# Optimization experiments

Measured on AMD Instinct MI355X. Metric: run time of the kernel, lower is better.

Reference implementation:

```python
import jax, jax.numpy as jnp
import numpy as np

B, CIN, COUT, H, W, K = 32, 256, 256, 56, 56, 3
STRIDE, PAD, DIL = 1, 1, 1
SPARSITY = 0.9  # fraction of weight entries pruned to zero


def setup_inputs() -> dict:
    key = jax.random.key(0)
    kx, kw, km = jax.random.split(key, 3)
    x = jax.random.normal(kx, (B, CIN, H, W), dtype=jnp.float32)
    w = jax.random.normal(kw, (COUT, CIN, K, K), dtype=jnp.float32)
    mask = (jax.random.uniform(km, (COUT, CIN, K, K)) > SPARSITY).astype(jnp.float32)
    w = w * mask
    return {"x": x, "weight": w}


def reference(x, weight):
    # Faithful math of SparseConv2D.forward (sparse path == nn.Conv2d, bias=None):
    # NCHW input, OIHW weight, stride/pad/dilation as configured.
    out = jax.lax.conv_general_dilated(
        x, weight,
        window_strides=(STRIDE, STRIDE),
        padding=[(PAD, PAD), (PAD, PAD)],
        rhs_dilation=(DIL, DIL),
        dimension_numbers=("NCHW", "OIHW", "NCHW"),
    )
    return out  # [B, COUT, H_out, W_out]
```

## Files before the change

### kernel.cpp

```cpp
#include <hip/hip_runtime.h>


typedef __attribute__((ext_vector_type(8))) short short8;
typedef __attribute__((ext_vector_type(4))) float f32x4;
typedef __attribute__((ext_vector_type(4))) int i32x4;

constexpr int BB = 32, CIN = 256, COUT = 256, H = 56, W = 56, HW = H * W;
constexpr int HP = 58, WP = 58;

constexpr size_t XP_ELEMS = (size_t)BB * HP * WP * CIN;
constexpr size_t WB_ELEMS = (size_t)COUT * 9 * CIN;
constexpr size_t WS_NEEDED = (XP_ELEMS + WB_ELEMS) * 2;

__device__ __forceinline__ ushort f2bf(float f) {
    unsigned x = __float_as_uint(f);
    unsigned r = (x + 0x7FFFu + ((x >> 16) & 1u)) >> 16;
    return (ushort)r;
}


__global__ __launch_bounds__(256)
void prep_xp(const float* __restrict__ x, ushort* __restrict__ xp) {
    const int bi = blockIdx.x;
    const int b = bi / HP, i = bi % HP;
    ushort* dst = xp + (size_t)bi * WP * CIN;
    const int tid = threadIdx.x;

    if (i == 0 || i == HP - 1) {
        i32x4 z = {0, 0, 0, 0};
        for (int k = tid; k < WP * CIN / 8; k += 256) ((i32x4*)dst)[k] = z;
        return;
    }

    __shared__ ushort t[W][CIN + 2];
    const int lane = tid & 63, wv = tid >> 6;
    if (lane < W) {
        const float* src = x + (size_t)b * CIN * HW + (size_t)(i - 1) * W + lane;
        for (int cin = wv; cin < CIN; cin += 4)
            t[lane][cin] = f2bf(src[(size_t)cin * HW]);
    }
    __syncthreads();
    for (int c = 0; c < WP; ++c)
        dst[c * CIN + tid] = (c == 0 || c == WP - 1) ? (ushort)0 : t[c - 1][tid];
}

__global__ __launch_bounds__(256)
void prep_wb2(const float* __restrict__ w, ushort* __restrict__ wb2) {
    const int d = blockIdx.x * 256 + threadIdx.x;
    const int ci = d & 31;
    const int cout = (d >> 5) & 255;
    const int r = d >> 13;
    const int tap = r % 9, cb = r / 9;
    const int cin = cb * 32 + ci;
    wb2[d] = f2bf(w[((size_t)cout * CIN + cin) * 9 + tap]);
}


#define SCHED_FENCE() __builtin_amdgcn_sched_barrier(0)
#define WAITV(N) asm volatile("s_waitcnt vmcnt(" #N ")" ::: "memory")

__device__ __forceinline__ void gload_lds16(const ushort* g, ushort* l) {
    __builtin_amdgcn_global_load_lds(
        (const __attribute__((address_space(1))) void*)g,
        (__attribute__((address_space(3))) void*)l, 16, 0, 0);
}


__global__ __launch_bounds__(256, 2)
void conv_mfma(const ushort* __restrict__ xp, const ushort* __restrict__ wb2,
               float* __restrict__ out) {
    int bx = blockIdx.x;
    bx = (bx & 7) * 112 + (bx >> 3);

    const int b  = bx / 28;
    const int p0 = (bx % 28) * 112;
    const int r0 = p0 / 56;

    const int tid  = threadIdx.x;
    const int wv   = tid >> 6;
    const int lane = tid & 63;
    const int ml   = lane & 15;
    const int g    = lane >> 4;

    __shared__ ushort As[2][1280 * 8];
    __shared__ ushort Xs[2][1280 * 8];

    int boff[7];
    #pragma unroll
    for (int nf = 0; nf < 7; ++nf) {
        const int p_  = p0 + nf * 16 + ml;
        const int hl  = (p_ >= p0 + 56) ? 1 : 0;
        const int col = p_ - 56 * (r0 + hl);
        boff[nf] = (hl * 58 + col) * 40 + 8 * g;
    }
    int aoff[4];
    #pragma unroll
    for (int mi = 0; mi < 4; ++mi)
        aoff[mi] = (64 * wv + 16 * mi + ml) * 40 + 8 * g;

    int goffA[5], goffX[5];
    #pragma unroll
    for (int k = 0; k < 5; ++k) {
        const int c = 256 * k + tid;
        const int s = c / 5, pc = c - s * 5;
        goffA[k] = (pc < 4) ? s * 32 + pc * 8 : 0;
        goffX[k] = (c < 1160 && pc < 4) ? s * 256 + pc * 8 : 0;
    }
    const size_t xbase = ((size_t)b * HP + r0) * WP * CIN;

    f32x4 acc[4][7] = {};

    #define STAGE_A(T, BUF)                                                     \
        { const ushort* _s = wb2 + (size_t)(T) * 8192;                          \
          _Pragma("unroll")                                                     \
          for (int k = 0; k < 5; ++k)                                           \
              gload_lds16(_s + goffA[k], &As[BUF][(256 * k + 64 * wv) * 8]);    \
        }
    #define STAGE_X(CB, BUF)                                                    \
        { const ushort* _s = xp + xbase + (CB) * 32;                            \
          _Pragma("unroll")                                                     \
          for (int k = 0; k < 5; ++k)                                           \
              gload_lds16(_s + goffX[k], &Xs[BUF][(256 * k + 64 * wv) * 8]);    \
        }

    STAGE_A(0, 0);
    STAGE_A(1, 1);
    STAGE_X(0, 0);
    WAITV(0);
    __builtin_amdgcn_s_barrier();

    #pragma unroll
    for (int cb = 0; cb < 8; ++cb) {
        #pragma unroll
        for (int tap = 0; tap < 9; ++tap) {
            const int t = cb * 9 + tap;

            if (t == 71)                      { WAITV(0); }
            else if (tap == 8 && cb < 7)      { WAITV(10); }
            else                              { WAITV(5);  }
            SCHED_FENCE();
            __builtin_amdgcn_s_barrier();
            SCHED_FENCE();

            const ushort* Ab = &As[t & 1][0];
            const ushort* Xb = &Xs[cb & 1][0];
            const int kh = tap / 3, kw = tap - kh * 3;
            const int toff = (kh * 58 + kw) * 40;

            short8 av[4], bv[7];
            #pragma unroll
            for (int mi = 0; mi < 4; ++mi) av[mi] = *(const short8*)(Ab + aoff[mi]);
            #pragma unroll
            for (int nf = 0; nf < 7; ++nf) bv[nf] = *(const short8*)(Xb + boff[nf] + toff);

            __builtin_amdgcn_s_setprio(1);
            #pragma unroll
            for (int mi = 0; mi < 4; ++mi)
                #pragma unroll
                for (int nf = 0; nf < 7; ++nf)
                    acc[mi][nf] = __builtin_amdgcn_mfma_f32_16x16x32_bf16(
                                      av[mi], bv[nf], acc[mi][nf], 0, 0, 0);
            __builtin_amdgcn_s_setprio(0);
            SCHED_FENCE();
            __builtin_amdgcn_s_barrier();
            SCHED_FENCE();

            if (t < 70) STAGE_A(t + 2, t & 1);
            if (tap == 7 && cb < 7) STAGE_X(cb + 1, (cb + 1) & 1);
            SCHED_FENCE();
        }
    }

    float* ob = out + (size_t)b * COUT * HW;
    #pragma unroll
    for (int mi = 0; mi < 4; ++mi)
        #pragma unroll
        for (int nf = 0; nf < 7; ++nf)
            #pragma unroll
            for (int r = 0; r < 4; ++r) {
                const int cout_l = 64 * wv + 16 * mi + 4 * g + r;
                const int p_ = p0 + 16 * nf + ml;
                ob[(size_t)cout_l * HW + p_] = acc[mi][nf][r];
            }
    #undef STAGE_A
    #undef STAGE_X
}


constexpr int WSZ = CIN * 9;
constexpr int NIN = 54 * 54;

__global__ __launch_bounds__(256)
void sparse_conv3x3(const float* __restrict__ x,
                    const float* __restrict__ wgt,
                    float* __restrict__ out) {
    const int bc = blockIdx.x, cout = bc % COUT, b = bc / COUT;
    const int tid = threadIdx.x;
    __shared__ int2 s_ent[WSZ];
    __shared__ unsigned char s_kk[WSZ];
    __shared__ int s_cnt[257];
    const float* wc = wgt + (size_t)cout * WSZ;
    float mv[9]; int cnt = 0;
    #pragma unroll
    for (int i = 0; i < 9; ++i) { mv[i] = wc[tid * 9 + i]; if (mv[i] != 0.0f) cnt++; }
    s_cnt[tid] = cnt; __syncthreads();
    if (tid == 0) { int run = 0; for (int t = 0; t < 256; ++t) { int c = s_cnt[t]; s_cnt[t] = run; run += c; } s_cnt[256] = run; }
    __syncthreads();
    { int pos = s_cnt[tid];
      #pragma unroll
      for (int i = 0; i < 9; ++i) if (mv[i] != 0.0f) {
          const int kh = i / 3, kw = i - kh * 3;
          int2 e; e.x = (tid * HW + (kh - 1) * W + (kw - 1)) * 4; e.y = __float_as_int(mv[i]);
          s_ent[pos] = e; s_kk[pos] = (unsigned char)(kh | (kw << 4)); pos++; } }
    __syncthreads();
    const int nnz = s_cnt[256];
    const char* xb = (const char*)(x + (size_t)b * CIN * HW);
    float* ob = out + (size_t)bc * HW;
    for (int o = tid; o < HW; o += 256) {
        int h, w; bool interior = (o < NIN);
        if (interior) { h = 1 + o / 54; w = 1 + (o - (h - 1) * 54); }
        else { int o2 = o - NIN;
            if (o2 < 56) { h = 0; w = o2; } else if (o2 < 112) { h = 55; w = o2 - 56; }
            else if (o2 < 166) { h = 1 + (o2 - 112); w = 0; } else { h = 1 + (o2 - 166); w = 55; } }
        const char* pb = xb + (size_t)(h * W + w) * 4;
        float acc = 0.0f;
        if (interior) {
            #pragma unroll 4
            for (int e = 0; e < nnz; ++e) { const int2 en = s_ent[e];
                acc = fmaf(__int_as_float(en.y), *(const float*)(pb + en.x), acc); }
        } else {
            const int h1 = h - 1, w1 = w - 1;
            for (int e = 0; e < nnz; ++e) { const int2 en = s_ent[e]; const int kk = s_kk[e];
                const int hh = h1 + (kk & 15), ww = w1 + (kk >> 4);
                if ((unsigned)hh < (unsigned)H && (unsigned)ww < (unsigned)W)
                    acc = fmaf(__int_as_float(en.y), *(const float*)(pb + en.x), acc); } }
        ob[h * W + w] = acc;
    }
}


extern "C" void kernel_launch(void* const* d_in, const int* in_sizes, int n_in,
                              void* d_out, int out_size, void* d_ws, size_t ws_size,
                              hipStream_t stream) {
    const float* x = (const float*)d_in[0];
    const float* w = (const float*)d_in[1];
    float* out = (float*)d_out;

    if (ws_size >= WS_NEEDED) {
        ushort* xp = (ushort*)d_ws;
        ushort* wbp = xp + XP_ELEMS;
        prep_xp<<<BB * HP, 256, 0, stream>>>(x, xp);
        prep_wb2<<<(int)(WB_ELEMS / 256), 256, 0, stream>>>(w, wbp);
        conv_mfma<<<896, 256, 0, stream>>>(xp, wbp, out);
    } else {
        sparse_conv3x3<<<BB * COUT, 256, 0, stream>>>(x, w, out);
    }
}
```

Before: 158.2 us.

## Triple-buffer weight tiles, XOR-swizzle LDS, and prefetch B fragments one tap ahead

Replaces the padded LDS layout (40-element row stride, five loads per stage) with a dense XOR-swizzled layout using four loads per stage, which is meant to avoid bank conflicts with less shared memory. Weight slabs become triple-buffered so each iteration needs one barrier instead of two, and input fragments for the next tap are read from LDS into registers before the current MFMAs are issued. The cost is more register pressure from the double-buffered B fragments, trickier vmcnt accounting, and wasted wraparound prefetches at the end of the loop.

```diff
diff --git a/kernel.cpp b/kernel.cpp
--- a/kernel.cpp
+++ b/kernel.cpp
@@ -57,7 +57,9 @@
 
 
 #define SCHED_FENCE() __builtin_amdgcn_sched_barrier(0)
-#define WAITV(N) asm volatile("s_waitcnt vmcnt(" #N ")" ::: "memory")
+#define WAITV0 asm volatile("s_waitcnt vmcnt(0)" ::: "memory")
+#define WAITV4 asm volatile("s_waitcnt vmcnt(4)" ::: "memory")
+#define WAITV8 asm volatile("s_waitcnt vmcnt(8)" ::: "memory")
 
 __device__ __forceinline__ void gload_lds16(const ushort* g, ushort* l) {
     __builtin_amdgcn_global_load_lds(
@@ -65,6 +67,7 @@
         (__attribute__((address_space(3))) void*)l, 16, 0, 0);
 }
 
+__device__ __forceinline__ int swz(int c) { return c ^ ((c >> 3) & 7); }
 
 __global__ __launch_bounds__(256, 2)
 void conv_mfma(const ushort* __restrict__ xp, const ushort* __restrict__ wb2,
@@ -82,76 +85,87 @@
     const int ml   = lane & 15;
     const int g    = lane >> 4;
 
-    __shared__ ushort As[2][1280 * 8];
-    __shared__ ushort Xs[2][1280 * 8];
-
-    int boff[7];
+    __shared__ ushort As[3][8192];
+    __shared__ ushort Xs[2][8192];
+
+    int aoffB[4];
+    #pragma unroll
+    for (int mi = 0; mi < 4; ++mi) {
+        const int c = (64 * wv + 16 * mi + ml) * 4 + g;
+        aoffB[mi] = swz(c) * 16;
+    }
+    int cbase[7];
     #pragma unroll
     for (int nf = 0; nf < 7; ++nf) {
-        const int p_  = p0 + nf * 16 + ml;
+        const int p_  = p0 + 16 * nf + ml;
         const int hl  = (p_ >= p0 + 56) ? 1 : 0;
         const int col = p_ - 56 * (r0 + hl);
-        boff[nf] = (hl * 58 + col) * 40 + 8 * g;
-    }
-    int aoff[4];
-    #pragma unroll
-    for (int mi = 0; mi < 4; ++mi)
-        aoff[mi] = (64 * wv + 16 * mi + ml) * 40 + 8 * g;
-
-    int goffA[5], goffX[5];
-    #pragma unroll
-    for (int k = 0; k < 5; ++k) {
-        const int c = 256 * k + tid;
-        const int s = c / 5, pc = c - s * 5;
-        goffA[k] = (pc < 4) ? s * 32 + pc * 8 : 0;
-        goffX[k] = (c < 1160 && pc < 4) ? s * 256 + pc * 8 : 0;
+        cbase[nf] = ((hl * 58 + col) * 4 + g);
+    }
+    int goffA[4], goffX[4];
+    #pragma unroll
+    for (int k = 0; k < 4; ++k) {
+        const int q = k * 256 + tid;
+        const int c = swz(q);
+        goffA[k] = (c >> 2) * 32 + (c & 3) * 8;
+        goffX[k] = (c < 928) ? ((c >> 2) * 256 + (c & 3) * 8) : 0;
     }
     const size_t xbase = ((size_t)b * HP + r0) * WP * CIN;
 
     f32x4 acc[4][7] = {};
-
-    #define STAGE_A(T, BUF)                                                     \
-        { const ushort* _s = wb2 + (size_t)(T) * 8192;                          \
+    short8 bvv[2][7];
+
+    #define STAGE_A(SLAB, BUF)                                                  \
+        { const ushort* _s = wb2 + (size_t)(SLAB) * 8192;                       \
           _Pragma("unroll")                                                     \
-          for (int k = 0; k < 5; ++k)                                           \
-              gload_lds16(_s + goffA[k], &As[BUF][(256 * k + 64 * wv) * 8]);    \
-        }
-    #define STAGE_X(CB, BUF)                                                    \
-        { const ushort* _s = xp + xbase + (CB) * 32;                            \
+          for (int k = 0; k < 4; ++k)                                           \
+              gload_lds16(_s + goffA[k], &As[BUF][(k * 256 + wv * 64) * 8]); }
+    #define STAGE_X(SLAB, BUF)                                                  \
+        { const ushort* _s = xp + xbase + (SLAB) * 32;                          \
           _Pragma("unroll")                                                     \
-          for (int k = 0; k < 5; ++k)                                           \
-              gload_lds16(_s + goffX[k], &Xs[BUF][(256 * k + 64 * wv) * 8]);    \
-        }
-
+          for (int k = 0; k < 4; ++k)                                           \
+              gload_lds16(_s + goffX[k], &Xs[BUF][(k * 256 + wv * 64) * 8]); }
+
+    STAGE_X(0, 0);
     STAGE_A(0, 0);
     STAGE_A(1, 1);
-    STAGE_X(0, 0);
-    WAITV(0);
-    __builtin_amdgcn_s_barrier();
-
-    #pragma unroll
-    for (int cb = 0; cb < 8; ++cb) {
+    WAITV4;
+    __syncthreads();
+    #pragma unroll
+    for (int nf = 0; nf < 7; ++nf)
+        bvv[0][nf] = *(const short8*)((const char*)&Xs[0][0] + swz(cbase[nf]) * 16);
+
+    const int DSLOT[9] = {0, 1, 2, 58, 59, 60, 116, 117, 118};
+
+    for (int j = 0; j < 4; ++j) {
         #pragma unroll
-        for (int tap = 0; tap < 9; ++tap) {
-            const int t = cb * 9 + tap;
-
-            if (t == 71)                      { WAITV(0); }
-            else if (tap == 8 && cb < 7)      { WAITV(10); }
-            else                              { WAITV(5);  }
-            SCHED_FENCE();
-            __builtin_amdgcn_s_barrier();
-            SCHED_FENCE();
-
-            const ushort* Ab = &As[t & 1][0];
-            const ushort* Xb = &Xs[cb & 1][0];
-            const int kh = tap / 3, kw = tap - kh * 3;
-            const int toff = (kh * 58 + kw) * 40;
-
-            short8 av[4], bv[7];
-            #pragma unroll
-            for (int mi = 0; mi < 4; ++mi) av[mi] = *(const short8*)(Ab + aoff[mi]);
-            #pragma unroll
-            for (int nf = 0; nf < 7; ++nf) bv[nf] = *(const short8*)(Xb + boff[nf] + toff);
+        for (int tt = 0; tt < 18; ++tt) {
+            const int tap  = tt % 9;
+            const int half = tt / 9;
+            if (tap == 8) { WAITV4; SCHED_FENCE(); }
+
+            int slab = 18 * j + tt + 2;
+            if (slab >= 72) slab -= 72;
+            STAGE_A(slab, (tt + 2) % 3);
+            if (tap == 6) {
+                int xsl = 2 * j + 1 + half;
+                if (xsl >= 8) xsl = 0;
+                STAGE_X(xsl, half ^ 1);
+            }
+
+            const ushort* Ab = &As[tt % 3][0];
+            short8 av[4];
+            #pragma unroll
+            for (int mi = 0; mi < 4; ++mi)
+                av[mi] = *(const short8*)((const char*)Ab + aoffB[mi]);
+            const int ntap = (tap == 8) ? 0 : (tap + 1);
+            const ushort* Xb = &Xs[(tap == 8) ? (half ^ 1) : half][0];
+            #pragma unroll
+            for (int nf = 0; nf < 7; ++nf) {
+                const int c = cbase[nf] + 4 * DSLOT[ntap];
+                bvv[(tt + 1) & 1][nf] =
+                    *(const short8*)((const char*)Xb + swz(c) * 16);
+            }
 
             __builtin_amdgcn_s_setprio(1);
             #pragma unroll
@@ -159,17 +173,16 @@
                 #pragma unroll
                 for (int nf = 0; nf < 7; ++nf)
                     acc[mi][nf] = __builtin_amdgcn_mfma_f32_16x16x32_bf16(
-                                      av[mi], bv[nf], acc[mi][nf], 0, 0, 0);
+                                      av[mi], bvv[tt & 1][nf], acc[mi][nf], 0, 0, 0);
             __builtin_amdgcn_s_setprio(0);
+            SCHED_FENCE();
+            if (tap == 6 || tap == 7) { WAITV8; } else { WAITV4; }
             SCHED_FENCE();
             __builtin_amdgcn_s_barrier();
             SCHED_FENCE();
-
-            if (t < 70) STAGE_A(t + 2, t & 1);
-            if (tap == 7 && cb < 7) STAGE_X(cb + 1, (cb + 1) & 1);
-            SCHED_FENCE();
         }
     }
+    WAITV0;
 
     float* ob = out + (size_t)b * COUT * HW;
     #pragma unroll
```

After: 210.2 us. 32.8% more time.
